# Performance work log

Measured on AMD Instinct MI355X. Metric: run time of the kernel, lower is better.

Reference implementation:

```python
import jax, jax.numpy as jnp
import numpy as np

B, N, DE, H, DH = 2, 1024, 1024, 16, 64
DK = H * DH  # total complex qkv dim per stream
MIN_EXP = -30.0
EPS = 1e-4


def setup_inputs():
    key = jax.random.key(0)
    ks = jax.random.split(key, 8)

    def g(i, shape, sc=1.0):
        return jax.random.normal(ks[i], shape, jnp.float32) * sc

    # RoPE-style per-head frequencies for the conjugate-paired half-dims
    freqs = 10000.0 ** (-np.arange(DH // 2, dtype=np.float64) / (DH // 2))
    omega = jnp.asarray(np.tile(freqs[None, :], (H, 1)), jnp.float32)
    return {
        "x": g(0, (B, N, DE)),
        "Wq": g(1, (DE, 2 * DK), 1.0 / np.sqrt(DE)),
        "Wk": g(2, (DE, 2 * DK), 1.0 / np.sqrt(DE)),
        "Wv": g(3, (DE, 2 * DK), 1.0 / np.sqrt(DE)),
        "Wo": g(4, (2 * DK, DE), 1.0 / np.sqrt(2 * DK)),
        "omega": omega,
        "mu_raw": g(5, (H,)) - 2.0,          # pre-sigmoid decay rates
        "sigma_raw": g(6, (H,)),              # pre-softplus process noise
        "eta_raw": jnp.ones((H,), jnp.float32),
        "gamma_raw": jnp.ones((H,), jnp.float32),
        "tau": jnp.ones((H,), jnp.float32),   # inverse temperature
        "nu_raw": jnp.ones((H,), jnp.float32) * 4.0,  # robustness dof
    }


def reference(x, Wq, Wk, Wv, Wo, omega, mu_raw, sigma_raw, eta_raw, gamma_raw, tau, nu_raw):
    B_, N_, _ = x.shape
    H_, d_half = omega.shape
    DH_ = 2 * d_half
    DKt = H_ * DH_

    def cproj(W):
        z = x @ W                          # [B,N,2D] real/imag packed
        D = W.shape[1] // 2
        zc = jax.lax.complex(z[..., :D], z[..., D:])
        return zc.reshape(B_, N_, H_, DH_)

    q, k, v = cproj(Wq), cproj(Wk), cproj(Wv)

    # complex-conjugate-constrained rotations: omega stacked as [w, -w]
    om = jnp.concatenate([omega, -omega], axis=-1)              # [H,DH]
    t = jnp.arange(N_, dtype=jnp.float32)
    ang = t[:, None, None] * om[None]                           # [N,H,DH]
    phase = jax.lax.complex(jnp.cos(ang), jnp.sin(ang))
    qr = q * phase[None]
    kr = k * phase[None]

    # isotropic SDE decay kernel  E_rel = exp(-mu * |t_i - t_j|)
    mu = jax.nn.sigmoid(mu_raw) + EPS                           # [H]
    dt = jnp.abs(t[:, None] - t[None, :])                       # [N,N]
    E = jnp.exp(jnp.clip(-mu[:, None, None] * dt[None], MIN_EXP, 0.0))  # [H,N,N]

    # Re<q_i, Phi(dt) k_j>  (rotation carried by phases, decay by E)
    s = jnp.einsum('bihd,bjhd->bhij', qr, jnp.conj(kr)).real    # [B,H,N,N]
    qn = (q.real ** 2 + q.imag ** 2).sum(-1).transpose(0, 2, 1)  # [B,H,N]
    kn = (k.real ** 2 + k.imag ** 2).sum(-1).transpose(0, 2, 1)

    # Lyapunov-propagated uncertainty: P(dt) = sigma^2/(2mu)(1 - E^2) + eta^2 + gamma^2
    sigma_sq = jax.nn.softplus(sigma_raw)
    eta_sq = jax.nn.softplus(eta_raw)
    gamma_sq = jax.nn.softplus(gamma_raw)
    V = (sigma_sq / (2.0 * mu))[:, None, None] * (1.0 - E * E) \
        + (eta_sq + gamma_sq)[:, None, None]                    # [H,N,N]

    # per-head Mahalanobis residual under the SDE forecast
    maha = jnp.maximum(qn[..., None] + (E * E)[None] * kn[:, :, None, :]
                       - 2.0 * E[None] * s, 0.0) / V[None]      # [B,H,N,N]

    # robust nu-thresholding (Student-t style) + Gaussian normalization term
    nu = jax.nn.softplus(nu_raw)
    coef = (-0.5 * tau * (nu + DH_))[None, :, None, None]
    logits = coef * jnp.log1p(maha / nu[None, :, None, None]) \
             - 0.5 * DH_ * jnp.log(V)[None]

    causal = (t[:, None] >= t[None, :])
    logits = jnp.where(causal[None, None], logits, -jnp.inf)
    A = jax.nn.softmax(logits, axis=-1)                         # [B,H,N,N]

    out = jnp.einsum('bhij,bjhd->bihd', A.astype(v.dtype), v)   # complex [B,N,H,DH]
    y = jnp.concatenate([out.real.reshape(B_, N_, DKt),
                         out.imag.reshape(B_, N_, DKt)], axis=-1)
    return y @ Wo                                               # [B,N,DE]
```

## Files before the change

kernel.cpp:

```cpp
#include <hip/hip_runtime.h>
#include <math.h>

#define BB      2
#define NN      1024
#define DE_     1024
#define HH      16
#define TWO_DK  2048
#define PK      4194304
#define TBLR    1092

typedef float f32x4  __attribute__((ext_vector_type(4)));
typedef short bf16x8 __attribute__((ext_vector_type(8)));

__device__ __forceinline__ short f2bf(float f) {
    unsigned u = __float_as_uint(f);
    unsigned r = (u + 0x7fffu + ((u >> 16) & 1u)) >> 16;
    return (short)r;
}
__device__ __forceinline__ float bf2f(short v) {
    return __uint_as_float(((unsigned)(unsigned short)v) << 16);
}

__device__ __forceinline__ float fexp2(float x) { return __builtin_amdgcn_exp2f(x); }
__device__ __forceinline__ float flog2(float x) { return __builtin_amdgcn_logf(x); }

#define GLDS16(g, l) __builtin_amdgcn_global_load_lds(                        \
    (const __attribute__((address_space(1))) unsigned int*)(g),               \
    (__attribute__((address_space(3))) unsigned int*)(l), 16, 0, 0)
#define GLDS4(g, l) __builtin_amdgcn_global_load_lds(                         \
    (const __attribute__((address_space(1))) unsigned int*)(g),               \
    (__attribute__((address_space(3))) unsigned int*)(l), 4, 0, 0)

__constant__ int jIT[24] = {7,14,15,15, 6,12,13,13,14, 5,10,11,11,12,
                            4, 8, 9, 9,10, 3, 8, 2, 1, 0};
__constant__ int jJ0[24] = {0, 0, 0, 8, 0, 0, 0, 7, 8, 0, 0, 0, 6, 7,
                            0, 0, 0, 5, 6, 0, 5, 0, 0, 0};
__constant__ int jJ1[24] = {7, 7, 7,15, 6, 6, 6,13,14, 5, 5, 5,11,12,
                            4, 4, 4, 9,10, 3, 8, 2, 1, 0};
__constant__ int jPS[24] = {0, 1, 1, 2, 0, 1, 1, 2, 2, 0, 1, 1, 2, 2,
                            0, 1, 1, 2, 2, 0, 2, 0, 0, 0};

__global__ __launch_bounds__(256) void prep(
    const float* __restrict__ x,
    const float* __restrict__ Wq, const float* __restrict__ Wk,
    const float* __restrict__ Wv, const float* __restrict__ Wo,
    const float* __restrict__ mu_raw, const float* __restrict__ sigma_raw,
    const float* __restrict__ eta_raw, const float* __restrict__ gamma_raw,
    short* __restrict__ xb, short* __restrict__ wt, short* __restrict__ wot,
    float4* __restrict__ tbl) {
    const int z = blockIdx.z;
    if (z == 4) {
        const int flat = blockIdx.y * 32 + blockIdx.x;
        const int i = (flat * 256 + threadIdx.x) * 8;
        float4 v0 = *(const float4*)&x[i];
        float4 v1 = *(const float4*)&x[i + 4];
        short4 o0, o1;
        o0.x = f2bf(v0.x); o0.y = f2bf(v0.y); o0.z = f2bf(v0.z); o0.w = f2bf(v0.w);
        o1.x = f2bf(v1.x); o1.y = f2bf(v1.y); o1.z = f2bf(v1.z); o1.w = f2bf(v1.w);
        *(short4*)&xb[i] = o0; *(short4*)&xb[i + 4] = o1;
        return;
    }
    if (z == 3 && blockIdx.x >= 16) {
        const int idx = blockIdx.y * 16 + (blockIdx.x - 16);
        if (idx >= 80) return;
        const int h = idx / 5, rb = idx % 5;
        const int r = rb * 256 + threadIdx.x;
        if (r >= TBLR) return;
        const float mu = 1.f / (1.f + expf(-mu_raw[h])) + 1e-4f;
        const float Ac = log1pf(expf(sigma_raw[h])) / (2.f * mu);
        const float Cc = log1pf(expf(eta_raw[h])) + log1pf(expf(gamma_raw[h]));
        const float arg = fminf(fmaxf(-mu * (float)(r - 64), -30.f), 0.f);
        const float E   = expf(arg);
        const float V   = fmaf(Ac, 1.f - E * E, Cc);
        tbl[h * TBLR + r] = make_float4(2.f * E, 1.f / V, -32.f * log2f(V), E * E);
        return;
    }
    const float* in; short* out; int R, C;
    if (z < 3) { if (blockIdx.y >= 16) return;
                 in = (z == 0) ? Wq : (z == 1) ? Wk : Wv;
                 out = wt + (size_t)z * 2097152; R = 1024; C = 2048; }
    else       { in = Wo; out = wot; R = 2048; C = 1024; }
    __shared__ float t[64][65];
    const int c0 = blockIdx.x * 64, r0 = blockIdx.y * 64;
    const int tr = threadIdx.x >> 4, tc4 = (threadIdx.x & 15) * 4;
#pragma unroll
    for (int s = 0; s < 4; ++s) {
        const int r = tr + s * 16;
        float4 v = *(const float4*)&in[(size_t)(r0 + r) * C + c0 + tc4];
        t[r][tc4] = v.x; t[r][tc4 + 1] = v.y; t[r][tc4 + 2] = v.z; t[r][tc4 + 3] = v.w;
    }
    __syncthreads();
#pragma unroll
    for (int s = 0; s < 4; ++s) {
        const int oc = tr + s * 16;
        short4 o;
        o.x = f2bf(t[tc4 + 0][oc]); o.y = f2bf(t[tc4 + 1][oc]);
        o.z = f2bf(t[tc4 + 2][oc]); o.w = f2bf(t[tc4 + 3][oc]);
        *(short4*)&out[(size_t)(c0 + oc) * R + r0 + tc4] = o;
    }
}

__global__ __launch_bounds__(256, 5) void gemm_qkv_rot2(
    const short* __restrict__ A, const short* __restrict__ wt,
    const float* __restrict__ omega,
    short* __restrict__ qb, short* __restrict__ kb, short* __restrict__ vtb,
    float* __restrict__ qn_, float* __restrict__ kn_) {
    __shared__ __align__(16) short As[64 * 64];
    __shared__ __align__(16) short Bs[128 * 64];
    __shared__ float sN[4][64];
    const int tid = threadIdx.x;
    const int m0  = blockIdx.x * 64;
    const int h   = blockIdx.y;
    const short* W = wt + (size_t)blockIdx.z * 2097152;

    const short* aP[2]; int aOff[2];
#pragma unroll
    for (int i = 0; i < 2; ++i) {
        const int c   = i * 256 + tid;
        const int row = c >> 3;
        const int src = ((c & 7) ^ (row & 7)) << 3;
        aOff[i] = c * 8;
        aP[i] = A + (size_t)(m0 + row) * 1024 + src;
    }
    const short* bP[4]; int bOff[4];
#pragma unroll
    for (int i = 0; i < 4; ++i) {
        const int c   = i * 256 + tid;
        const int row = c >> 3;
        const int src = ((c & 7) ^ (row & 7)) << 3;
        bOff[i] = c * 8;
        const int t_ = row >> 5, u_ = (row >> 4) & 1, dcol = t_ * 16 + (row & 15);
        bP[i] = W + (size_t)(u_ * 1024 + h * 64 + dcol) * 1024 + src;
    }

    const int lane = tid & 63, w = tid >> 6;
    const int wc = w * 32;
    const int fr = lane & 15;
    const int fo = (lane >> 4) << 3;
    const int sw = (fr & 7) << 3;

    f32x4 acc[4][2];
#pragma unroll
    for (int a = 0; a < 4; ++a)
#pragma unroll
        for (int b = 0; b < 2; ++b) acc[a][b] = (f32x4){0.f, 0.f, 0.f, 0.f};

    for (int k0 = 0; k0 < 1024; k0 += 64) {
#pragma unroll
        for (int i = 0; i < 2; ++i) GLDS16(aP[i] + k0, &As[aOff[i]]);
#pragma unroll
        for (int i = 0; i < 4; ++i) GLDS16(bP[i] + k0, &Bs[bOff[i]]);
        __syncthreads();
#pragma unroll
        for (int ks = 0; ks < 64; ks += 32) {
            bf16x8 af[4], bf[2];
#pragma unroll
            for (int a = 0; a < 4; ++a)
                af[a] = *(const bf16x8*)&As[(a * 16 + fr) * 64 + ((ks + fo) ^ sw)];
#pragma unroll
            for (int b = 0; b < 2; ++b)
                bf[b] = *(const bf16x8*)&Bs[(wc + b * 16 + fr) * 64 + ((ks + fo) ^ sw)];
#pragma unroll
            for (int a = 0; a < 4; ++a)
#pragma unroll
                for (int b = 0; b < 2; ++b)
                    acc[a][b] = __builtin_amdgcn_mfma_f32_16x16x32_bf16(
                        af[a], bf[b], acc[a][b], 0, 0, 0);
        }
        __syncthreads();
    }

    const int quad = lane >> 4, cq = quad * 4, l15 = lane & 15;
    const int bh  = (m0 >> 10) * 16 + h;
    const int nb0 = (m0 & 1023) + cq;

    if (blockIdx.z == 2) {
#pragma unroll
        for (int a = 0; a < 4; ++a) {
#pragma unroll
            for (int b = 0; b < 2; ++b) {
                const int cl = wc + b * 16;
                const int dd = ((cl >> 4) & 1) * 64 + (cl >> 5) * 16 + l15;
                short4 o;
                o.x = f2bf(acc[a][b][0]); o.y = f2bf(acc[a][b][1]);
                o.z = f2bf(acc[a][b][2]); o.w = f2bf(acc[a][b][3]);
                *(short4*)&vtb[((size_t)bh * 128 + dd) * 1024 + nb0 + a * 16] = o;
            }
        }
        return;
    }
    float* nout = (blockIdx.z == 0) ? qn_ : kn_;
    short* obuf = (blockIdx.z == 0) ? qb  : kb;

#pragma unroll
    for (int a = 0; a < 4; ++a) {
        float ns[4] = {0.f, 0.f, 0.f, 0.f};
#pragma unroll
        for (int b = 0; b < 2; ++b)
#pragma unroll
            for (int r = 0; r < 4; ++r)
                ns[r] = fmaf(acc[a][b][r], acc[a][b][r], ns[r]);
#pragma unroll
        for (int m2 = 1; m2 < 16; m2 <<= 1)
#pragma unroll
            for (int r = 0; r < 4; ++r) ns[r] += __shfl_xor(ns[r], m2);
        if (l15 == 0)
#pragma unroll
            for (int r = 0; r < 4; ++r) sN[w][a * 16 + cq + r] = ns[r];
    }
    __syncthreads();
    if (tid < 64)
        nout[(size_t)bh * 1024 + (m0 & 1023) + tid] =
            sN[0][tid] + sN[1][tid] + sN[2][tid] + sN[3][tid];

    {
        const int d = w * 16 + l15;
        const float om = (d < 32) ? omega[h * 32 + d] : -omega[h * 32 + d - 32];
#pragma unroll
        for (int a = 0; a < 4; ++a) {
#pragma unroll
            for (int r = 0; r < 4; ++r) {
                const int n2 = nb0 + a * 16 + r;
                float sn, cs;
                __sincosf((float)n2 * om, &sn, &cs);
                const float re = acc[a][0][r], im = acc[a][1][r];
                short* orow = obuf + ((size_t)bh * 1024 + n2) * 128;
                orow[d]      = f2bf(re * cs - im * sn);
                orow[64 + d] = f2bf(re * sn + im * cs);
            }
        }
    }
}

__global__ __launch_bounds__(256) void attn_mfma(
    const short* __restrict__ qr, const short* __restrict__ kr,
    const short* __restrict__ vt,
    const float* __restrict__ qn, const float* __restrict__ kn,
    const float4* __restrict__ tbl,
    const float* __restrict__ tau_p, const float* __restrict__ nu_raw,
    short* __restrict__ y, short* __restrict__ po0, float* __restrict__ pml) {
    __shared__ __align__(16) short Ks[2][64 * 128];
    __shared__ __align__(16) short Vs[2][128 * 64];
    __shared__ __align__(16) short Ps[64 * 72];
    __shared__ __align__(16) float4 sT[2][128];
    __shared__ float sKn[2][64];

    const int bx   = blockIdx.x;
    const int xcd  = bx & 7;
    const int rest = bx >> 3;
    const int jrk  = rest >> 2;
    const int bh   = xcd * 4 + (rest & 3);
    const int h    = bh & 15;
    const int it   = jIT[jrk];
    const int j0j  = jJ0[jrk];
    const int j1j  = jJ1[jrk];
    const int psel = jPS[jrk];
    const int i0   = it * 64;
    const int pq   = bh * 8 + (it - 8);

    const int tid  = threadIdx.x;
    const int lane = tid & 63, w = tid >> 6;
    const int quad = lane >> 4, l15 = lane & 15;

    const float nu     = log1pf(expf(nu_raw[h]));
    const float coef   = -0.5f * tau_p[h] * (nu + 64.0f);
    const float inv_nu = 1.f / nu;

    const short* Qb  = qr + (size_t)bh * NN * 128;
    const short* Kb  = kr + (size_t)bh * NN * 128;
    const short* Vtb = vt + (size_t)bh * 128 * NN;

#define STAGE(JT, P) do {                                                     \
        const int j0_ = (JT) * 64, dt0_ = i0 - j0_;                           \
        _Pragma("unroll")                                                     \
        for (int i_ = 0; i_ < 4; ++i_) {                                      \
            const int c_ = i_ * 256 + tid, row_ = c_ >> 4;                    \
            const int src_ = ((c_ & 15) ^ (row_ & 7)) * 8;                    \
            GLDS16(Kb + (size_t)(j0_ + row_) * 128 + src_, &Ks[P][c_ * 8]);   \
        }                                                                     \
        _Pragma("unroll")                                                     \
        for (int i_ = 0; i_ < 4; ++i_) {                                      \
            const int c_ = i_ * 256 + tid, d_ = c_ >> 3;                      \
            const int src_ = ((c_ & 7) ^ (d_ & 7)) * 8;                       \
            GLDS16(Vtb + (size_t)d_ * NN + j0_ + src_, &Vs[P][c_ * 8]);       \
        }                                                                     \
        if (w == 0) {                                                         \
            GLDS16(tbl + h * TBLR + 1 + dt0_ + lane, &sT[P][lane]);           \
            GLDS16(tbl + h * TBLR + 65 + dt0_ + lane, &sT[P][64 + lane]);     \
        } else if (w == 1) {                                                  \
            GLDS4(kn + (size_t)bh * NN + j0_ + lane, &sKn[P][lane]);          \
        }                                                                     \
    } while (0)

    bf16x8 qf[4];
    const int arow = i0 + w * 16 + l15;
#pragma unroll
    for (int ks = 0; ks < 4; ++ks)
        qf[ks] = *(const bf16x8*)&Qb[(size_t)arow * 128 + ks * 32 + quad * 8];

    float mrow[4];
    f32x4 o[8];
    f32x4 o9 = (f32x4){0.f, 0.f, 0.f, 0.f};
#pragma unroll
    for (int r = 0; r < 4; ++r) mrow[r] = -INFINITY;
#pragma unroll
    for (int s = 0; s < 8; ++s) o[s] = (f32x4){0.f, 0.f, 0.f, 0.f};
    float qn4[4];
#pragma unroll
    for (int r = 0; r < 4; ++r)
        qn4[r] = qn[(size_t)bh * NN + i0 + w * 16 + quad * 4 + r];

    const bf16x8 onesv = (bf16x8){0x3F80, 0x3F80, 0x3F80, 0x3F80,
                                  0x3F80, 0x3F80, 0x3F80, 0x3F80};

    STAGE(j0j, 0);
    __syncthreads();

    for (int jt = j0j; jt <= j1j; ++jt) {
        const int p = (jt - j0j) & 1;
        if (jt < j1j) STAGE(jt + 1, 1 - p);

        f32x4 sAcc[4];
#pragma unroll
        for (int s = 0; s < 4; ++s) sAcc[s] = (f32x4){0.f, 0.f, 0.f, 0.f};
#pragma unroll
        for (int ks = 0; ks < 4; ++ks) {
#pragma unroll
            for (int s = 0; s < 4; ++s) {
                const int brow = s * 16 + l15;
                bf16x8 bK = *(const bf16x8*)&Ks[p][brow * 128 +
                                                  (((ks * 4 + quad) ^ (brow & 7)) * 8)];
                sAcc[s] = __builtin_amdgcn_mfma_f32_16x16x32_bf16(qf[ks], bK, sAcc[s], 0, 0, 0);
            }
        }

        float al[4];
        bool anyr = false;
#pragma unroll
        for (int r = 0; r < 4; ++r) {
            const int row = w * 16 + quad * 4 + r;
            float lg[4];
#pragma unroll
            for (int s = 0; s < 4; ++s) {
                const int col = s * 16 + l15;
                const float4 T = sT[p][row - col + 63];
                const float sv = sAcc[s][r];
                const float t1 = fmaf(T.w, sKn[p][col], qn4[r]);
                const float maha = fmaxf(fmaf(-T.x, sv, t1), 0.f) * T.y;
                float v = fmaf(coef, flog2(fmaf(maha, inv_nu, 1.f)), T.z);
                if (jt == it && col > row) v = -INFINITY;
                lg[s] = v;
            }
            float mx = fmaxf(fmaxf(lg[0], lg[1]), fmaxf(lg[2], lg[3]));
            mx = fmaxf(mx, __shfl_xor(mx, 1));
            mx = fmaxf(mx, __shfl_xor(mx, 2));
            mx = fmaxf(mx, __shfl_xor(mx, 4));
            mx = fmaxf(mx, __shfl_xor(mx, 8));
            const bool resc = mx > mrow[r] + 16.f;
            const float mu_ = resc ? mx : mrow[r];
            al[r] = resc ? fexp2(mrow[r] - mx) : 1.f;
            mrow[r] = mu_;
            anyr = anyr || resc;
#pragma unroll
            for (int s = 0; s < 4; ++s) {
                const float pv = fexp2(lg[s] - mu_);
                Ps[row * 72 + s * 16 + l15] = f2bf(pv);
            }
        }
        if (anyr) {
#pragma unroll
            for (int s = 0; s < 8; ++s)
#pragma unroll
                for (int r = 0; r < 4; ++r) o[s][r] *= al[r];
#pragma unroll
            for (int r = 0; r < 4; ++r) o9[r] *= al[r];
        }

#pragma unroll
        for (int jc = 0; jc < 2; ++jc) {
            bf16x8 aP = *(const bf16x8*)&Ps[(w * 16 + l15) * 72 + jc * 32 + quad * 8];
#pragma unroll
            for (int sub = 0; sub < 8; ++sub) {
                const int d = sub * 16 + l15;
                bf16x8 bV = *(const bf16x8*)&Vs[p][d * 64 + (((jc * 4 + quad) ^ (d & 7)) * 8)];
                o[sub] = __builtin_amdgcn_mfma_f32_16x16x32_bf16(aP, bV, o[sub], 0, 0, 0);
            }
            o9 = __builtin_amdgcn_mfma_f32_16x16x32_bf16(aP, onesv, o9, 0, 0, 0);
        }
        if (jt < j1j) __syncthreads();
    }
#undef STAGE

    short* dst = (psel == 1) ? po0 : y;
    const size_t rbase = (psel == 1) ? (size_t)pq * 64 : ((size_t)bh * NN + i0);
#pragma unroll
    for (int r = 0; r < 4; ++r) {
        const int lrow = w * 16 + quad * 4 + r;
        const float inv = 1.f / o9[r];
        const size_t base = (rbase + lrow) * 128;
#pragma unroll
        for (int sub = 0; sub < 8; ++sub)
            dst[base + sub * 16 + l15] = f2bf(o[sub][r] * inv);
        if (psel != 0 && l15 == 0)
            pml[(pq * 2 + (psel - 1)) * 64 + lrow] = mrow[r] + flog2(o9[r]);
    }
}

__global__ __launch_bounds__(256) void attn_merge(
    const short* __restrict__ po0, const float* __restrict__ pml,
    short* __restrict__ y) {
    const int qs = blockIdx.x;
    const int bh = qs >> 3, it = (qs & 7) + 8;
    const int t = threadIdx.x;
    const int row = t >> 2, dc = (t & 3) * 32;
    const float m1 = pml[(qs * 2 + 0) * 64 + row];
    const float m2 = pml[(qs * 2 + 1) * 64 + row];
    const float mx = fmaxf(m1, m2);
    const float w1 = fexp2(m1 - mx), w2 = fexp2(m2 - mx);
    const float inv = 1.f / (w1 + w2);
    const float a = w1 * inv, b = w2 * inv;
    const short* s1 = po0 + ((size_t)qs * 64 + row) * 128 + dc;
    short*       s2 = y + ((size_t)bh * NN + it * 64 + row) * 128 + dc;
#pragma unroll
    for (int i = 0; i < 32; i += 8) {
        bf16x8 v1 = *(const bf16x8*)(s1 + i);
        bf16x8 v2 = *(const bf16x8*)(s2 + i);
        bf16x8 ov;
#pragma unroll
        for (int k = 0; k < 8; ++k)
            ov[k] = f2bf(a * bf2f(v1[k]) + b * bf2f(v2[k]));
        *(bf16x8*)(s2 + i) = ov;
    }
}

__global__ __launch_bounds__(256) void gemm_out64(
    const short* __restrict__ yb, const short* __restrict__ wot,
    float* __restrict__ out) {
    __shared__ __align__(16) short As[2][64 * 64];
    __shared__ __align__(16) short Bs[2][64 * 64];
    const int tid = threadIdx.x;
    const int m0  = blockIdx.x * 64;
    const int n0  = blockIdx.y * 64;
    const int bb  = m0 >> 10;

    int aPre[2], aOff[2]; const short* bP[2];
#pragma unroll
    for (int i = 0; i < 2; ++i) {
        const int c = i * 256 + tid, row = c >> 3;
        const int src = ((c & 7) ^ (row & 7)) << 3;
        aPre[i] = ((m0 & 1023) + row) * 128 + src;
        bP[i] = wot + (size_t)(n0 + row) * 2048 + src;
        aOff[i] = c * 8;
    }

    const int lane = tid & 63, w = tid >> 6;
    const int wr = (w >> 1) * 32, wc = (w & 1) * 32;
    const int fr = lane & 15;
    const int fo = (lane >> 4) << 3;
    const int sw = (fr & 7) << 3;

    f32x4 acc[2][2];
#pragma unroll
    for (int a = 0; a < 2; ++a)
#pragma unroll
        for (int b = 0; b < 2; ++b) acc[a][b] = (f32x4){0.f, 0.f, 0.f, 0.f};

#define OSTAGE(KT, P) do {                                                    \
        const int k0_ = (KT) * 64;                                            \
        const int hh_ = (k0_ >> 6) & 15, im_ = k0_ >> 10;                     \
        const short* ab_ = yb + ((size_t)(bb * 16 + hh_) << 17) + im_ * 64;   \
        _Pragma("unroll")                                                     \
        for (int i_ = 0; i_ < 2; ++i_) GLDS16(ab_ + aPre[i_], &As[P][aOff[i_]]); \
        _Pragma("unroll")                                                     \
        for (int i_ = 0; i_ < 2; ++i_) GLDS16(bP[i_] + k0_, &Bs[P][aOff[i_]]);   \
    } while (0)

    OSTAGE(0, 0);
    __syncthreads();

    for (int kt = 0; kt < 32; ++kt) {
        const int p = kt & 1;
        if (kt < 31) OSTAGE(kt + 1, 1 - p);
#pragma unroll
        for (int ks = 0; ks < 64; ks += 32) {
            bf16x8 af[2], bf[2];
#pragma unroll
            for (int a = 0; a < 2; ++a)
                af[a] = *(const bf16x8*)&As[p][(wr + a * 16 + fr) * 64 + ((ks + fo) ^ sw)];
#pragma unroll
            for (int b = 0; b < 2; ++b)
                bf[b] = *(const bf16x8*)&Bs[p][(wc + b * 16 + fr) * 64 + ((ks + fo) ^ sw)];
#pragma unroll
            for (int a = 0; a < 2; ++a)
#pragma unroll
                for (int b = 0; b < 2; ++b)
                    acc[a][b] = __builtin_amdgcn_mfma_f32_16x16x32_bf16(
                        af[a], bf[b], acc[a][b], 0, 0, 0);
        }
        if (kt < 31) __syncthreads();
    }
#undef OSTAGE

    const int cq = (lane >> 4) * 4, l15 = lane & 15;
#pragma unroll
    for (int a = 0; a < 2; ++a)
#pragma unroll
        for (int b = 0; b < 2; ++b)
#pragma unroll
            for (int r = 0; r < 4; ++r)
                out[(size_t)(m0 + wr + a * 16 + cq + r) * 1024 +
                    (n0 + wc + b * 16 + l15)] = acc[a][b][r];
}

extern "C" void kernel_launch(void* const* d_in, const int* in_sizes, int n_in,
                              void* d_out, int out_size, void* d_ws, size_t ws_size,
                              hipStream_t stream) {
    const float* x         = (const float*)d_in[0];
    const float* Wq        = (const float*)d_in[1];
    const float* Wk        = (const float*)d_in[2];
    const float* Wv        = (const float*)d_in[3];
    const float* Wo        = (const float*)d_in[4];
    const float* omega     = (const float*)d_in[5];
    const float* mu_raw    = (const float*)d_in[6];
    const float* sigma_raw = (const float*)d_in[7];
    const float* eta_raw   = (const float*)d_in[8];
    const float* gamma_raw = (const float*)d_in[9];
    const float* tau       = (const float*)d_in[10];
    const float* nu_raw    = (const float*)d_in[11];
    float* out = (float*)d_out;

    short*  qb  = (short*)d_ws;
    short*  kb  = qb + PK;
    short*  vtb = kb + PK;
    float*  qn  = (float*)(vtb + PK);
    float*  kn  = qn + 32768;
    float4* tbl = (float4*)(kn + 32768);
    short*  wot = (short*)(tbl + HH * TBLR);
    short*  wt  = wot + 2097152;
    short*  xb  = wt + 3 * 2097152;
    short*  yb  = wt;
    short*  po0 = wt + 4194304;
    float*  pml = (float*)xb;

    prep<<<dim3(32, 32, 5), 256, 0, stream>>>(
        x, Wq, Wk, Wv, Wo, mu_raw, sigma_raw, eta_raw, gamma_raw,
        xb, wt, wot, tbl);
    gemm_qkv_rot2<<<dim3(32, 16, 3), 256, 0, stream>>>(
        xb, wt, omega, qb, kb, vtb, qn, kn);
    attn_mfma<<<dim3(768), 256, 0, stream>>>(
        qb, kb, vtb, qn, kn, tbl, tau, nu_raw, yb, po0, pml);
    attn_merge<<<dim3(256), 256, 0, stream>>>(po0, pml, yb);
    gemm_out64<<<dim3(32, 16), 256, 0, stream>>>(yb, wot, out);
}
```

Before: 200.0 us.

## Single-buffer attention LDS tiles and double the out-projection K tile

The attention kernel drops double-buffering of its K, V, decay-table and key-norm tiles in shared memory. It now loads each tile and synchronises before computing on it, which roughly halves its LDS footprint so more blocks can be resident per CU. The cost is losing the overlap of the next tile's global loads with the current tile's compute. The output GEMM now stages two 64-wide K chunks per step (128 total), halving the number of loop iterations and barriers at the price of more LDS per block.

```diff
diff --git a/kernel.cpp b/kernel.cpp
--- a/kernel.cpp
+++ b/kernel.cpp
@@ -239,11 +239,11 @@
     const float4* __restrict__ tbl,
     const float* __restrict__ tau_p, const float* __restrict__ nu_raw,
     short* __restrict__ y, short* __restrict__ po0, float* __restrict__ pml) {
-    __shared__ __align__(16) short Ks[2][64 * 128];
-    __shared__ __align__(16) short Vs[2][128 * 64];
+    __shared__ __align__(16) short Ks[64 * 128];
+    __shared__ __align__(16) short Vs[128 * 64];
     __shared__ __align__(16) short Ps[64 * 72];
-    __shared__ __align__(16) float4 sT[2][128];
-    __shared__ float sKn[2][64];
+    __shared__ __align__(16) float4 sT[128];
+    __shared__ float sKn[64];
 
     const int bx   = blockIdx.x;
     const int xcd  = bx & 7;
@@ -270,25 +270,25 @@
     const short* Kb  = kr + (size_t)bh * NN * 128;
     const short* Vtb = vt + (size_t)bh * 128 * NN;
 
-#define STAGE(JT, P) do {                                                     \
+#define STAGE(JT) do {                                                        \
         const int j0_ = (JT) * 64, dt0_ = i0 - j0_;                           \
         _Pragma("unroll")                                                     \
         for (int i_ = 0; i_ < 4; ++i_) {                                      \
             const int c_ = i_ * 256 + tid, row_ = c_ >> 4;                    \
             const int src_ = ((c_ & 15) ^ (row_ & 7)) * 8;                    \
-            GLDS16(Kb + (size_t)(j0_ + row_) * 128 + src_, &Ks[P][c_ * 8]);   \
+            GLDS16(Kb + (size_t)(j0_ + row_) * 128 + src_, &Ks[c_ * 8]);      \
         }                                                                     \
         _Pragma("unroll")                                                     \
         for (int i_ = 0; i_ < 4; ++i_) {                                      \
             const int c_ = i_ * 256 + tid, d_ = c_ >> 3;                      \
             const int src_ = ((c_ & 7) ^ (d_ & 7)) * 8;                       \
-            GLDS16(Vtb + (size_t)d_ * NN + j0_ + src_, &Vs[P][c_ * 8]);       \
+            GLDS16(Vtb + (size_t)d_ * NN + j0_ + src_, &Vs[c_ * 8]);          \
         }                                                                     \
         if (w == 0) {                                                         \
-            GLDS16(tbl + h * TBLR + 1 + dt0_ + lane, &sT[P][lane]);           \
-            GLDS16(tbl + h * TBLR + 65 + dt0_ + lane, &sT[P][64 + lane]);     \
+            GLDS16(tbl + h * TBLR + 1 + dt0_ + lane, &sT[lane]);              \
+            GLDS16(tbl + h * TBLR + 65 + dt0_ + lane, &sT[64 + lane]);        \
         } else if (w == 1) {                                                  \
-            GLDS4(kn + (size_t)bh * NN + j0_ + lane, &sKn[P][lane]);          \
+            GLDS4(kn + (size_t)bh * NN + j0_ + lane, &sKn[lane]);             \
         }                                                                     \
     } while (0)
 
@@ -313,12 +313,9 @@
     const bf16x8 onesv = (bf16x8){0x3F80, 0x3F80, 0x3F80, 0x3F80,
                                   0x3F80, 0x3F80, 0x3F80, 0x3F80};
 
-    STAGE(j0j, 0);
-    __syncthreads();
-
     for (int jt = j0j; jt <= j1j; ++jt) {
-        const int p = (jt - j0j) & 1;
-        if (jt < j1j) STAGE(jt + 1, 1 - p);
+        STAGE(jt);
+        __syncthreads();
 
         f32x4 sAcc[4];
 #pragma unroll
@@ -328,8 +325,8 @@
 #pragma unroll
             for (int s = 0; s < 4; ++s) {
                 const int brow = s * 16 + l15;
-                bf16x8 bK = *(const bf16x8*)&Ks[p][brow * 128 +
-                                                  (((ks * 4 + quad) ^ (brow & 7)) * 8)];
+                bf16x8 bK = *(const bf16x8*)&Ks[brow * 128 +
+                                                (((ks * 4 + quad) ^ (brow & 7)) * 8)];
                 sAcc[s] = __builtin_amdgcn_mfma_f32_16x16x32_bf16(qf[ks], bK, sAcc[s], 0, 0, 0);
             }
         }
@@ -343,9 +340,9 @@
 #pragma unroll
             for (int s = 0; s < 4; ++s) {
                 const int col = s * 16 + l15;
-                const float4 T = sT[p][row - col + 63];
+                const float4 T = sT[row - col + 63];
                 const float sv = sAcc[s][r];
-                const float t1 = fmaf(T.w, sKn[p][col], qn4[r]);
+                const float t1 = fmaf(T.w, sKn[col], qn4[r]);
                 const float maha = fmaxf(fmaf(-T.x, sv, t1), 0.f) * T.y;
                 float v = fmaf(coef, flog2(fmaf(maha, inv_nu, 1.f)), T.z);
                 if (jt == it && col > row) v = -INFINITY;
@@ -382,7 +379,7 @@
 #pragma unroll
             for (int sub = 0; sub < 8; ++sub) {
                 const int d = sub * 16 + l15;
-                bf16x8 bV = *(const bf16x8*)&Vs[p][d * 64 + (((jc * 4 + quad) ^ (d & 7)) * 8)];
+                bf16x8 bV = *(const bf16x8*)&Vs[d * 64 + (((jc * 4 + quad) ^ (d & 7)) * 8)];
                 o[sub] = __builtin_amdgcn_mfma_f32_16x16x32_bf16(aP, bV, o[sub], 0, 0, 0);
             }
             o9 = __builtin_amdgcn_mfma_f32_16x16x32_bf16(aP, onesv, o9, 0, 0, 0);
@@ -436,8 +433,8 @@
 __global__ __launch_bounds__(256) void gemm_out64(
     const short* __restrict__ yb, const short* __restrict__ wot,
     float* __restrict__ out) {
-    __shared__ __align__(16) short As[2][64 * 64];
-    __shared__ __align__(16) short Bs[2][64 * 64];
+    __shared__ __align__(16) short As[2][2 * 64 * 64];
+    __shared__ __align__(16) short Bs[2][2 * 64 * 64];
     const int tid = threadIdx.x;
     const int m0  = blockIdx.x * 64;
     const int n0  = blockIdx.y * 64;
@@ -466,30 +463,36 @@
         for (int b = 0; b < 2; ++b) acc[a][b] = (f32x4){0.f, 0.f, 0.f, 0.f};
 
 #define OSTAGE(KT, P) do {                                                    \
-        const int k0_ = (KT) * 64;                                            \
-        const int hh_ = (k0_ >> 6) & 15, im_ = k0_ >> 10;                     \
-        const short* ab_ = yb + ((size_t)(bb * 16 + hh_) << 17) + im_ * 64;   \
         _Pragma("unroll")                                                     \
-        for (int i_ = 0; i_ < 2; ++i_) GLDS16(ab_ + aPre[i_], &As[P][aOff[i_]]); \
-        _Pragma("unroll")                                                     \
-        for (int i_ = 0; i_ < 2; ++i_) GLDS16(bP[i_] + k0_, &Bs[P][aOff[i_]]);   \
+        for (int hf_ = 0; hf_ < 2; ++hf_) {                                   \
+            const int k0_ = (KT) * 128 + hf_ * 64;                            \
+            const int hh_ = (k0_ >> 6) & 15, im_ = k0_ >> 10;                 \
+            const short* ab_ = yb + ((size_t)(bb * 16 + hh_) << 17) + im_ * 64; \
+            _Pragma("unroll")                                                 \
+            for (int i_ = 0; i_ < 2; ++i_)                                    \
+                GLDS16(ab_ + aPre[i_], &As[P][hf_ * 4096 + aOff[i_]]);        \
+            _Pragma("unroll")                                                 \
+            for (int i_ = 0; i_ < 2; ++i_)                                    \
+                GLDS16(bP[i_] + k0_, &Bs[P][hf_ * 4096 + aOff[i_]]);          \
+        }                                                                     \
     } while (0)
 
     OSTAGE(0, 0);
     __syncthreads();
 
-    for (int kt = 0; kt < 32; ++kt) {
+    for (int kt = 0; kt < 16; ++kt) {
         const int p = kt & 1;
-        if (kt < 31) OSTAGE(kt + 1, 1 - p);
-#pragma unroll
-        for (int ks = 0; ks < 64; ks += 32) {
+        if (kt < 15) OSTAGE(kt + 1, 1 - p);
+#pragma unroll
+        for (int ks = 0; ks < 128; ks += 32) {
+            const int hb = (ks >> 6) * 4096, kk = ks & 63;
             bf16x8 af[2], bf[2];
 #pragma unroll
             for (int a = 0; a < 2; ++a)
-                af[a] = *(const bf16x8*)&As[p][(wr + a * 16 + fr) * 64 + ((ks + fo) ^ sw)];
+                af[a] = *(const bf16x8*)&As[p][hb + (wr + a * 16 + fr) * 64 + ((kk + fo) ^ sw)];
 #pragma unroll
             for (int b = 0; b < 2; ++b)
-                bf[b] = *(const bf16x8*)&Bs[p][(wc + b * 16 + fr) * 64 + ((ks + fo) ^ sw)];
+                bf[b] = *(const bf16x8*)&Bs[p][hb + (wc + b * 16 + fr) * 64 + ((kk + fo) ^ sw)];
 #pragma unroll
             for (int a = 0; a < 2; ++a)
 #pragma unroll
@@ -497,7 +500,7 @@
                     acc[a][b] = __builtin_amdgcn_mfma_f32_16x16x32_bf16(
                         af[a], bf[b], acc[a][b], 0, 0, 0);
         }
-        if (kt < 31) __syncthreads();
+        if (kt < 15) __syncthreads();
     }
 #undef OSTAGE
 
```

New measurement: 192.2 us, median of 2. 1.04x faster.
